# Optimization experiments

Hardware: AMD Instinct MI355X
Metric: run time of the kernel (lower is better)

The kernel has to match this reference:

```python
import jax, jax.numpy as jnp
import numpy as np

N = 100000   # nodes
E = 1600000  # edges
F = 128      # node_feature_dim
H = 128      # hidden_dim
O = 256      # output_dim
G = 256      # number of graphs in the batch


def setup_inputs() -> dict:
    key = jax.random.key(0)
    ks = jax.random.split(key, 12)
    x = jax.random.normal(ks[0], (N, F), dtype=jnp.float32)
    edge_index = jax.random.randint(ks[1], (2, E), 0, N, dtype=jnp.int64)
    batch = jnp.sort(jax.random.randint(ks[2], (N,), 0, G, dtype=jnp.int64))

    def lin(k, fan_in, shape):
        return (jax.random.normal(k, shape, dtype=jnp.float32) / np.float32(np.sqrt(fan_in)))

    W1 = lin(ks[3], F, (F, H)); b1 = jnp.zeros((H,), jnp.float32)
    W2 = lin(ks[4], H, (H, H)); b2 = jnp.zeros((H,), jnp.float32)
    W3 = lin(ks[5], H, (H, H)); b3 = jnp.zeros((H,), jnp.float32)
    Wfc = lin(ks[6], H, (H, O))
    bfc = lin(ks[7], H, (O,))
    return {"x": x, "W1": W1, "b1": b1, "W2": W2, "b2": b2,
            "W3": W3, "b3": b3, "Wfc": Wfc, "bfc": bfc,
            "edge_index": edge_index, "batch": batch}


def _gcn_norm(edge_index, n_nodes):
    # PyG GCNConv default: add self-loops, symmetric normalization.
    loop = jnp.arange(n_nodes, dtype=edge_index.dtype)
    row = jnp.concatenate([edge_index[0], loop])  # source
    col = jnp.concatenate([edge_index[1], loop])  # target
    deg = jax.ops.segment_sum(jnp.ones_like(col, dtype=jnp.float32), col,
                              num_segments=n_nodes)
    dinv = jnp.where(deg > 0, jax.lax.rsqrt(deg), 0.0)
    norm = dinv[row] * dinv[col]  # [E+N]
    return row, col, norm


def _gcn_conv(x, W, b, row, col, norm, n_nodes):
    h = x @ W                                   # transform first (PyG order)
    msg = norm[:, None] * h[row]                # gather + scale
    out = jax.ops.segment_sum(msg, col, num_segments=n_nodes)  # scatter-add
    return out + b


def reference(x, W1, b1, W2, b2, W3, b3, Wfc, bfc, edge_index, batch):
    n_nodes = x.shape[0]
    row, col, norm = _gcn_norm(edge_index, n_nodes)
    h = jax.nn.relu(_gcn_conv(x, W1, b1, row, col, norm, n_nodes))
    h = jax.nn.relu(_gcn_conv(h, W2, b2, row, col, norm, n_nodes))
    h = jax.nn.relu(_gcn_conv(h, W3, b3, row, col, norm, n_nodes))
    # global_mean_pool over graph ids
    sums = jax.ops.segment_sum(h, batch, num_segments=G)
    cnt = jax.ops.segment_sum(jnp.ones((n_nodes,), jnp.float32), batch,
                              num_segments=G)
    pooled = sums / jnp.maximum(cnt, 1.0)[:, None]
    return pooled @ Wfc + bfc
```

## Files before the change

### kernel.cpp

```cpp
#include <hip/hip_runtime.h>

#define NF 128
#define NH 128
#define NO 256
#define NG 256

typedef unsigned int   u32;
typedef unsigned short u16;
typedef __attribute__((ext_vector_type(8))) short short8;
typedef __attribute__((ext_vector_type(4))) float floatx4;

__device__ __forceinline__ float bflo(u32 g) { return __uint_as_float(g << 16); }
__device__ __forceinline__ float bfhi(u32 g) { return __uint_as_float(g & 0xffff0000u); }
__device__ __forceinline__ u16 f2bf(float x) {
    u32 u = __float_as_uint(x);
    u += 0x7fffu + ((u >> 16) & 1u);
    return (u16)(u >> 16);
}
__device__ __forceinline__ u32 packbf2(float x, float y) {
    u32 ux = __float_as_uint(x); ux += 0x7fffu + ((ux >> 16) & 1u);
    u32 uy = __float_as_uint(y); uy += 0x7fffu + ((uy >> 16) & 1u);
    return (ux >> 16) | (uy & 0xffff0000u);
}


__global__ __launch_bounds__(256) void count_coarse(const int* __restrict__ col, int E,
                                                    int* __restrict__ bucketCnt) {
    __shared__ int h[256];
    int t = threadIdx.x;
    h[t] = 0;
    __syncthreads();
    int base = blockIdx.x * 4096;
    #pragma unroll
    for (int i = 0; i < 16; ++i) {
        int e = base + i * 256 + t;
        if (e < E) atomicAdd(&h[col[e] >> 9], 1);
    }
    __syncthreads();
    if (h[t]) atomicAdd(&bucketCnt[t], h[t]);
}

__global__ void scan_buckets(const int* __restrict__ bucketCnt, int* __restrict__ cbase,
                             int* __restrict__ gcur) {
    __shared__ int sh[256];
    int t = threadIdx.x;
    int v = bucketCnt[t];
    sh[t] = v; __syncthreads();
    for (int d = 1; d < 256; d <<= 1) {
        int x = (t >= d) ? sh[t - d] : 0;
        __syncthreads();
        sh[t] += x;
        __syncthreads();
    }
    cbase[t] = sh[t] - v;
    gcur[t]  = sh[t] - v;
}


__global__ __launch_bounds__(256) void bin_coarse(const int* __restrict__ row,
                                                  const int* __restrict__ col,
                                                  int* __restrict__ gcur,
                                                  u32* __restrict__ coarse, int E) {
    __shared__ u32 cnt[256];
    __shared__ u32 lcur[256];
    __shared__ u32 gbase[256];
    __shared__ u32 sc[256];
    __shared__ u32 packed[4096];
    int t = threadIdx.x;
    int base = blockIdx.x * 4096;
    cnt[t] = 0;
    __syncthreads();

    u32 rv[16], cv[16];
    #pragma unroll
    for (int i = 0; i < 16; ++i) {
        int e = base + i * 256 + t;
        if (e < E) {
            rv[i] = (u32)row[e];
            cv[i] = (u32)col[e];
            atomicAdd(&cnt[cv[i] >> 9], 1u);
        }
    }
    __syncthreads();
    u32 own = cnt[t];
    sc[t] = own; __syncthreads();
    for (int d = 1; d < 256; d <<= 1) {
        u32 x = (t >= d) ? sc[t - d] : 0;
        __syncthreads();
        sc[t] += x;
        __syncthreads();
    }
    u32 excl = sc[t] - own;
    u32 total = sc[255];
    if (own > 0) gbase[t] = (u32)atomicAdd(&gcur[t], (int)own);
    cnt[t]  = excl;
    lcur[t] = excl;
    __syncthreads();

    #pragma unroll
    for (int i = 0; i < 16; ++i) {
        int e = base + i * 256 + t;
        if (e < E) {
            u32 p = atomicAdd(&lcur[cv[i] >> 9], 1u);
            packed[p] = rv[i] | ((cv[i] & 511u) << 17);
        }
    }
    __syncthreads();

    for (u32 i = t; i < total; i += 256) {
        u32 lo = 0, hi = 255;
        while (lo < hi) { u32 mid = (lo + hi + 1) >> 1; if (cnt[mid] <= i) lo = mid; else hi = mid - 1; }
        coarse[gbase[lo] + (i - cnt[lo])] = packed[i];
    }
}


__global__ __launch_bounds__(256) void build_csr_bucket(const u32* __restrict__ coarse,
                                                        const int* __restrict__ cbase,
                                                        const int* __restrict__ bucketCnt,
                                                        u32* __restrict__ srcs,
                                                        int* __restrict__ deg,
                                                        float* __restrict__ dinv,
                                                        int* __restrict__ offs, int N) {
    __shared__ u32 buf[10240];
    __shared__ u32 hist[512];
    __shared__ u32 scn[512];
    __shared__ u32 tmp[512];
    __shared__ u32 cur[512];
    int t = threadIdx.x;
    int b = blockIdx.x;
    int lo = b << 9;
    if (lo >= N) return;
    int cnt  = bucketCnt[b];
    int base = cbase[b];

    for (int j = t; j < 512; j += 256) hist[j] = 0;
    __syncthreads();
    for (int i = t; i < cnt; i += 256) {
        u32 pk = coarse[base + i];
        buf[i] = pk;
        atomicAdd(&hist[pk >> 17], 1u);
    }
    __syncthreads();
    for (int j = t; j < 512; j += 256) scn[j] = hist[j];
    __syncthreads();
    for (int d = 1; d < 512; d <<= 1) {
        for (int j = t; j < 512; j += 256) tmp[j] = (j >= d) ? scn[j - d] : 0u;
        __syncthreads();
        for (int j = t; j < 512; j += 256) scn[j] += tmp[j];
        __syncthreads();
    }
    int hi = min(lo + 512, N) - lo;
    for (int j = t; j < 512; j += 256) {
        u32 excl = scn[j] - hist[j];
        cur[j] = excl;
        if (j < hi) {
            deg[lo + j]  = (int)hist[j];
            dinv[lo + j] = rsqrtf((float)hist[j] + 1.0f);
            offs[lo + j] = base + (int)excl;
        }
    }
    __syncthreads();
    for (int i = t; i < cnt; i += 256) {
        u32 pk = buf[i];
        u32 c = pk >> 17;
        u32 p = atomicAdd(&cur[c], 1u);
        srcs[base + p] = pk & 0x1ffffu;
    }
}


__global__ void cast_w_t3(const float* __restrict__ W1, const float* __restrict__ W2,
                          const float* __restrict__ W3, u16* __restrict__ Wt1,
                          u16* __restrict__ Wt2, u16* __restrict__ Wt3) {
    int idx = blockIdx.x * 256 + threadIdx.x;
    int w = idx >> 14;
    int r = idx & 16383;
    const float* W = (w == 0) ? W1 : (w == 1) ? W2 : W3;
    u16* Wt = (w == 0) ? Wt1 : (w == 1) ? Wt2 : Wt3;
    int k = r >> 7, c = r & 127;
    Wt[c * NF + k] = f2bf(W[r]);
}


__device__ __forceinline__ void gemm_body(u16* As, u16* Wt, const u16* Wtg,
                                          const float* dinv, u16* C, int n,
                                          int node0, int t) {
    const uint4* Wg = (const uint4*)Wtg;
    #pragma unroll
    for (int i = 0; i < 8; ++i) {
        int idx = t + 256 * i;
        int cc = idx >> 4, q = idx & 15;
        *(uint4*)&Wt[cc * 136 + q * 8] = Wg[cc * 16 + q];
    }
    __syncthreads();

    int wv = t >> 6;
    int l  = t & 63;
    int lr = l & 15;
    int lq = l >> 4;

    floatx4 acc[8];
    #pragma unroll
    for (int c = 0; c < 8; ++c) acc[c] = (floatx4){0.f, 0.f, 0.f, 0.f};

    #pragma unroll
    for (int kk = 0; kk < 4; ++kk) {
        short8 af = *(const short8*)&As[(wv * 16 + lr) * 136 + kk * 32 + lq * 8];
        #pragma unroll
        for (int c = 0; c < 8; ++c) {
            short8 bf = *(const short8*)&Wt[(c * 16 + lr) * 136 + kk * 32 + lq * 8];
            acc[c] = __builtin_amdgcn_mfma_f32_16x16x32_bf16(af, bf, acc[c], 0, 0, 0);
        }
    }
    __syncthreads();

    float* Cs = (float*)Wt;
    #pragma unroll
    for (int c = 0; c < 8; ++c)
        #pragma unroll
        for (int r = 0; r < 4; ++r)
            Cs[(wv * 16 + lq * 4 + r) * 132 + c * 16 + lr] = acc[c][r];
    __syncthreads();

    int nd = t >> 2, seg = t & 3;
    if (node0 + nd < n) {
        float di = dinv[node0 + nd];
        const float* src = &Cs[nd * 132 + seg * 32];
        u32 o[16];
        #pragma unroll
        for (int i = 0; i < 16; ++i) o[i] = packbf2(di * src[2 * i], di * src[2 * i + 1]);
        uint4* dst = (uint4*)(C + (size_t)(node0 + nd) * NH + seg * 32);
        dst[0] = make_uint4(o[0],  o[1],  o[2],  o[3]);
        dst[1] = make_uint4(o[4],  o[5],  o[6],  o[7]);
        dst[2] = make_uint4(o[8],  o[9],  o[10], o[11]);
        dst[3] = make_uint4(o[12], o[13], o[14], o[15]);
    }
}

__global__ __launch_bounds__(256) void gemm_mfma(const u16* __restrict__ A,
                                                 const u16* __restrict__ Wtg,
                                                 const float* __restrict__ dinv,
                                                 u16* __restrict__ C, int n) {
    __shared__ u16 As[64 * 136];
    __shared__ u16 Wt[128 * 136];
    int t = threadIdx.x;
    int node0 = blockIdx.x * 64;

    const uint4* Ag = (const uint4*)A;
    #pragma unroll
    for (int i = 0; i < 4; ++i) {
        int idx = t + 256 * i;
        int nd = idx >> 4, q = idx & 15;
        uint4 v = make_uint4(0, 0, 0, 0);
        if (node0 + nd < n) v = Ag[(size_t)(node0 + nd) * 16 + q];
        *(uint4*)&As[nd * 136 + q * 8] = v;
    }
    gemm_body(As, Wt, Wtg, dinv, C, n, node0, t);
}

__global__ __launch_bounds__(256) void gemm_mfma_f32(const float* __restrict__ A,
                                                     const u16* __restrict__ Wtg,
                                                     const float* __restrict__ dinv,
                                                     u16* __restrict__ C, int n) {
    __shared__ u16 As[64 * 136];
    __shared__ u16 Wt[128 * 136];
    int t = threadIdx.x;
    int node0 = blockIdx.x * 64;

    const float4* Ag = (const float4*)A;
    #pragma unroll
    for (int i = 0; i < 8; ++i) {
        int idx = t + 256 * i;
        int nd = idx >> 5, q = idx & 31;
        float4 v = make_float4(0.f, 0.f, 0.f, 0.f);
        if (node0 + nd < n) v = Ag[(size_t)(node0 + nd) * 32 + q];
        uint2 p; p.x = packbf2(v.x, v.y); p.y = packbf2(v.z, v.w);
        *(uint2*)&As[nd * 136 + q * 4] = p;
    }
    gemm_body(As, Wt, Wtg, dinv, C, n, node0, t);
}


__global__ __launch_bounds__(256) void gcn_aggregate(const u16* __restrict__ gtab,
                                                     const u32* __restrict__ srcs,
                                                     const int* __restrict__ offs,
                                                     const int* __restrict__ deg,
                                                     const float* __restrict__ dinv,
                                                     const float* __restrict__ bias,
                                                     u16* __restrict__ outb, int n) {
    int wv = threadIdx.x >> 6;
    int l  = threadIdx.x & 63;
    int node = blockIdx.x * 4 + wv;
    if (node >= n) return;
    int start = offs[node];
    int end   = start + deg[node];
    const u32* rows = (const u32*)gtab;

    float a0 = 0.f, a1 = 0.f;
    int k = start;
    for (; k + 16 <= end; k += 16) {
        u32 gv[16];
        #pragma unroll
        for (int i = 0; i < 16; ++i) {
            u32 s = srcs[k + i];
            gv[i] = rows[(size_t)s * 64 + l];
        }
        #pragma unroll
        for (int i = 0; i < 16; ++i) { a0 += bflo(gv[i]); a1 += bfhi(gv[i]); }
    }
    for (; k + 4 <= end; k += 4) {
        u32 s0 = srcs[k], s1 = srcs[k + 1], s2 = srcs[k + 2], s3 = srcs[k + 3];
        u32 g0 = rows[(size_t)s0 * 64 + l];
        u32 g1 = rows[(size_t)s1 * 64 + l];
        u32 g2 = rows[(size_t)s2 * 64 + l];
        u32 g3 = rows[(size_t)s3 * 64 + l];
        a0 += bflo(g0) + bflo(g1) + bflo(g2) + bflo(g3);
        a1 += bfhi(g0) + bfhi(g1) + bfhi(g2) + bfhi(g3);
    }
    for (; k < end; ++k) {
        u32 g = rows[(size_t)srcs[k] * 64 + l];
        a0 += bflo(g); a1 += bfhi(g);
    }
    u32 gs = rows[(size_t)node * 64 + l];
    a0 += bflo(gs); a1 += bfhi(gs);
    float di = dinv[node];
    float2 bb = *(const float2*)&bias[l * 2];
    a0 = fmaxf(di * a0 + bb.x, 0.f);
    a1 = fmaxf(di * a1 + bb.y, 0.f);
    ((u32*)outb)[(size_t)node * 64 + l] = packbf2(a0, a1);
}


__global__ __launch_bounds__(256) void pool_partial(const u16* __restrict__ h,
                                                    const int* __restrict__ batch,
                                                    float* __restrict__ pooled, int n) {
    int t = threadIdx.x;
    int j = t & 127, half = t >> 7;
    int bs = blockIdx.x * 128;
    int be = min(bs + 128, n);
    float acc = 0.f;
    int cur = -1;
    for (int i = bs + half; i < be; i += 2) {
        int g = batch[i];
        if (g != cur) {
            if (cur >= 0) atomicAdd(&pooled[(size_t)cur * NH + j], acc);
            acc = 0.f; cur = g;
        }
        acc += __uint_as_float((u32)h[(size_t)i * NH + j] << 16);
    }
    if (cur >= 0) atomicAdd(&pooled[(size_t)cur * NH + j], acc);
}


__global__ __launch_bounds__(256) void final_fc(const float* __restrict__ pooled,
                                                const int* __restrict__ batch,
                                                const float* __restrict__ Wfc,
                                                const float* __restrict__ bfc,
                                                float* __restrict__ out, int n) {
    int g = blockIdx.x;
    int tid = threadIdx.x;

    int lo = 0, hi = n;
    while (lo < hi) { int m = (lo + hi) >> 1; if (batch[m] < g) lo = m + 1; else hi = m; }
    int start = lo;
    hi = n;
    while (lo < hi) { int m = (lo + hi) >> 1; if (batch[m] < g + 1) lo = m + 1; else hi = m; }
    int end = lo;

    __shared__ float pr[NH];
    float inv = 1.0f / fmaxf((float)(end - start), 1.0f);
    if (tid < NH) pr[tid] = pooled[(size_t)g * NH + tid] * inv;
    __syncthreads();

    float o = bfc[tid];
    #pragma unroll 8
    for (int k = 0; k < NH; ++k) o += pr[k] * Wfc[(size_t)k * NO + tid];
    out[(size_t)g * NO + tid] = o;
}


extern "C" void kernel_launch(void* const* d_in, const int* in_sizes, int n_in,
                              void* d_out, int out_size, void* d_ws, size_t ws_size,
                              hipStream_t stream) {
    const float* x   = (const float*)d_in[0];
    const float* W1  = (const float*)d_in[1];
    const float* b1  = (const float*)d_in[2];
    const float* W2  = (const float*)d_in[3];
    const float* b2  = (const float*)d_in[4];
    const float* W3  = (const float*)d_in[5];
    const float* b3  = (const float*)d_in[6];
    const float* Wfc = (const float*)d_in[7];
    const float* bfc = (const float*)d_in[8];
    const int*   ei  = (const int*)d_in[9];
    const int*   bat = (const int*)d_in[10];
    float* out = (float*)d_out;

    const int N = in_sizes[0] / NF;
    const int E = in_sizes[9] / 2;
    const int* rowp = ei;
    const int* colp = ei + E;

    char* w = (char*)d_ws;
    u32* srcs    = (u32*)w;                      w += (size_t)E * 4;
    u32* coarse  = (u32*)w;                      w += (size_t)E * 4;
    u16* hA   = (u16*)w;                         w += (size_t)N * NH * 2;
    u16* hB   = (u16*)w;                         w += (size_t)N * NH * 2;
    u16* tmpb = (u16*)w;                         w += (size_t)N * NH * 2;
    u16* Wt1  = (u16*)w;                         w += NF * NH * 2;
    u16* Wt2  = (u16*)w;                         w += NF * NH * 2;
    u16* Wt3  = (u16*)w;                         w += NF * NH * 2;
    float* dinv = (float*)w;                     w += (size_t)N * 4;
    int* degc   = (int*)w;                       w += (size_t)N * 4;
    int* offs   = (int*)w;                       w += (size_t)N * 4;
    float* pooled = (float*)w;                   w += (size_t)NG * NH * 4;
    int* bucketCnt = (int*)w;                    w += 256 * 4;
    int* cbase  = (int*)w;                       w += 256 * 4;
    int* gcur   = (int*)w;                       w += 256 * 4;

    const int TB = 256;
    int gGemm = (N + 63) / 64;
    int gAgg  = (N + 3) / 4;
    int gPool = (N + 127) / 128;
    int NB = (N + 511) >> 9;
    int gBin = (E + 4095) / 4096;

    hipMemsetAsync(pooled, 0, (size_t)NG * NH * 4 + 256 * 4, stream);

    count_coarse<<<gBin, TB, 0, stream>>>(colp, E, bucketCnt);
    scan_buckets<<<1, 256, 0, stream>>>(bucketCnt, cbase, gcur);
    bin_coarse<<<gBin, TB, 0, stream>>>(rowp, colp, gcur, coarse, E);
    build_csr_bucket<<<NB, TB, 0, stream>>>(coarse, cbase, bucketCnt, srcs, degc, dinv, offs, N);

    cast_w_t3<<<192, TB, 0, stream>>>(W1, W2, W3, Wt1, Wt2, Wt3);

    gemm_mfma_f32<<<gGemm, TB, 0, stream>>>(x, Wt1, dinv, tmpb, N);
    gcn_aggregate<<<gAgg, TB, 0, stream>>>(tmpb, srcs, offs, degc, dinv, b1, hB, N);

    gemm_mfma<<<gGemm, TB, 0, stream>>>(hB, Wt2, dinv, tmpb, N);
    gcn_aggregate<<<gAgg, TB, 0, stream>>>(tmpb, srcs, offs, degc, dinv, b2, hA, N);

    gemm_mfma<<<gGemm, TB, 0, stream>>>(hA, Wt3, dinv, tmpb, N);
    gcn_aggregate<<<gAgg, TB, 0, stream>>>(tmpb, srcs, offs, degc, dinv, b3, hB, N);

    pool_partial<<<gPool, TB, 0, stream>>>(hB, bat, pooled, N);
    final_fc<<<NG, NO, 0, stream>>>(pooled, bat, Wfc, bfc, out, N);
}
```

Baseline: 462.1 us.

## Use persistent GEMM blocks with resident weights and merge setup kernels

The GEMM kernels become persistent. A capped grid of blocks loads the transposed bf16 weight tile into shared memory once, then loops over node tiles, and the epilogue reuses the A buffer in two halves. The weight cast kernel is folded into the edge-count kernel, and zeroing of the pooled buffer moves into the scan kernel, cutting launches and memsets. This is meant to avoid reloading weights per 64-node tile and to reduce launch overhead. The cost is less parallelism per launch and extra barriers per tile.

```diff
diff --git a/kernel.cpp b/kernel.cpp
--- a/kernel.cpp
+++ b/kernel.cpp
@@ -24,13 +24,29 @@
 }
 
 
-__global__ __launch_bounds__(256) void count_coarse(const int* __restrict__ col, int E,
+__global__ __launch_bounds__(256) void setup_kernel(const float* __restrict__ W1,
+                                                    const float* __restrict__ W2,
+                                                    const float* __restrict__ W3,
+                                                    u16* __restrict__ Wt1, u16* __restrict__ Wt2,
+                                                    u16* __restrict__ Wt3,
+                                                    const int* __restrict__ col, int E,
                                                     int* __restrict__ bucketCnt) {
+    int b = blockIdx.x;
+    int t = threadIdx.x;
+    if (b < 192) {
+        int idx = b * 256 + t;
+        int w = idx >> 14;
+        int r = idx & 16383;
+        const float* W = (w == 0) ? W1 : (w == 1) ? W2 : W3;
+        u16* Wt = (w == 0) ? Wt1 : (w == 1) ? Wt2 : Wt3;
+        int k = r >> 7, c = r & 127;
+        Wt[c * NF + k] = f2bf(W[r]);
+        return;
+    }
     __shared__ int h[256];
-    int t = threadIdx.x;
     h[t] = 0;
     __syncthreads();
-    int base = blockIdx.x * 4096;
+    int base = (b - 192) * 4096;
     #pragma unroll
     for (int i = 0; i < 16; ++i) {
         int e = base + i * 256 + t;
@@ -41,7 +57,7 @@
 }
 
 __global__ void scan_buckets(const int* __restrict__ bucketCnt, int* __restrict__ cbase,
-                             int* __restrict__ gcur) {
+                             int* __restrict__ gcur, float* __restrict__ pooled) {
     __shared__ int sh[256];
     int t = threadIdx.x;
     int v = bucketCnt[t];
@@ -54,6 +70,10 @@
     }
     cbase[t] = sh[t] - v;
     gcur[t]  = sh[t] - v;
+    float4 z = make_float4(0.f, 0.f, 0.f, 0.f);
+    float4* p4 = (float4*)pooled;
+    #pragma unroll
+    for (int i = 0; i < 32; ++i) p4[i * 256 + t] = z;
 }
 
 
@@ -170,31 +190,8 @@
 }
 
 
-__global__ void cast_w_t3(const float* __restrict__ W1, const float* __restrict__ W2,
-                          const float* __restrict__ W3, u16* __restrict__ Wt1,
-                          u16* __restrict__ Wt2, u16* __restrict__ Wt3) {
-    int idx = blockIdx.x * 256 + threadIdx.x;
-    int w = idx >> 14;
-    int r = idx & 16383;
-    const float* W = (w == 0) ? W1 : (w == 1) ? W2 : W3;
-    u16* Wt = (w == 0) ? Wt1 : (w == 1) ? Wt2 : Wt3;
-    int k = r >> 7, c = r & 127;
-    Wt[c * NF + k] = f2bf(W[r]);
-}
-
-
-__device__ __forceinline__ void gemm_body(u16* As, u16* Wt, const u16* Wtg,
-                                          const float* dinv, u16* C, int n,
-                                          int node0, int t) {
-    const uint4* Wg = (const uint4*)Wtg;
-    #pragma unroll
-    for (int i = 0; i < 8; ++i) {
-        int idx = t + 256 * i;
-        int cc = idx >> 4, q = idx & 15;
-        *(uint4*)&Wt[cc * 136 + q * 8] = Wg[cc * 16 + q];
-    }
-    __syncthreads();
-
+__device__ __forceinline__ void gemm_tile(u16* As, const u16* Wt, const float* dinv,
+                                          u16* C, int n, int node0, int t) {
     int wv = t >> 6;
     int l  = t & 63;
     int lr = l & 15;
@@ -213,72 +210,99 @@
             acc[c] = __builtin_amdgcn_mfma_f32_16x16x32_bf16(af, bf, acc[c], 0, 0, 0);
         }
     }
-    __syncthreads();
-
-    float* Cs = (float*)Wt;
-    #pragma unroll
-    for (int c = 0; c < 8; ++c)
-        #pragma unroll
-        for (int r = 0; r < 4; ++r)
-            Cs[(wv * 16 + lq * 4 + r) * 132 + c * 16 + lr] = acc[c][r];
-    __syncthreads();
-
-    int nd = t >> 2, seg = t & 3;
-    if (node0 + nd < n) {
-        float di = dinv[node0 + nd];
-        const float* src = &Cs[nd * 132 + seg * 32];
-        u32 o[16];
-        #pragma unroll
-        for (int i = 0; i < 16; ++i) o[i] = packbf2(di * src[2 * i], di * src[2 * i + 1]);
-        uint4* dst = (uint4*)(C + (size_t)(node0 + nd) * NH + seg * 32);
-        dst[0] = make_uint4(o[0],  o[1],  o[2],  o[3]);
-        dst[1] = make_uint4(o[4],  o[5],  o[6],  o[7]);
-        dst[2] = make_uint4(o[8],  o[9],  o[10], o[11]);
-        dst[3] = make_uint4(o[12], o[13], o[14], o[15]);
-    }
+
+    float* Cs = (float*)As;
+    #pragma unroll
+    for (int h = 0; h < 2; ++h) {
+        __syncthreads();
+        if ((wv >> 1) == h) {
+            int lrow = (wv & 1) * 16 + lq * 4;
+            #pragma unroll
+            for (int c = 0; c < 8; ++c)
+                #pragma unroll
+                for (int r = 0; r < 4; ++r)
+                    Cs[(lrow + r) * 132 + c * 16 + lr] = acc[c][r];
+        }
+        __syncthreads();
+        int nd = t >> 3, seg = t & 7;
+        int node = node0 + h * 32 + nd;
+        if (node < n) {
+            float di = dinv[node];
+            const float* src = &Cs[nd * 132 + seg * 16];
+            u32 o[8];
+            #pragma unroll
+            for (int i = 0; i < 8; ++i) o[i] = packbf2(di * src[2 * i], di * src[2 * i + 1]);
+            uint4* dst = (uint4*)(C + (size_t)node * NH + seg * 16);
+            dst[0] = make_uint4(o[0], o[1], o[2], o[3]);
+            dst[1] = make_uint4(o[4], o[5], o[6], o[7]);
+        }
+    }
+    __syncthreads();
 }
 
 __global__ __launch_bounds__(256) void gemm_mfma(const u16* __restrict__ A,
                                                  const u16* __restrict__ Wtg,
                                                  const float* __restrict__ dinv,
-                                                 u16* __restrict__ C, int n) {
+                                                 u16* __restrict__ C, int n, int ntiles) {
+    __shared__ u16 Wt[128 * 136];
     __shared__ u16 As[64 * 136];
-    __shared__ u16 Wt[128 * 136];
-    int t = threadIdx.x;
-    int node0 = blockIdx.x * 64;
-
-    const uint4* Ag = (const uint4*)A;
-    #pragma unroll
-    for (int i = 0; i < 4; ++i) {
+    int t = threadIdx.x;
+
+    const uint4* Wg = (const uint4*)Wtg;
+    #pragma unroll
+    for (int i = 0; i < 8; ++i) {
         int idx = t + 256 * i;
-        int nd = idx >> 4, q = idx & 15;
-        uint4 v = make_uint4(0, 0, 0, 0);
-        if (node0 + nd < n) v = Ag[(size_t)(node0 + nd) * 16 + q];
-        *(uint4*)&As[nd * 136 + q * 8] = v;
-    }
-    gemm_body(As, Wt, Wtg, dinv, C, n, node0, t);
+        int cc = idx >> 4, q = idx & 15;
+        *(uint4*)&Wt[cc * 136 + q * 8] = Wg[cc * 16 + q];
+    }
+
+    for (int tile = blockIdx.x; tile < ntiles; tile += gridDim.x) {
+        int node0 = tile * 64;
+        const uint4* Ag = (const uint4*)A;
+        #pragma unroll
+        for (int i = 0; i < 4; ++i) {
+            int idx = t + 256 * i;
+            int nd = idx >> 4, q = idx & 15;
+            uint4 v = make_uint4(0, 0, 0, 0);
+            if (node0 + nd < n) v = Ag[(size_t)(node0 + nd) * 16 + q];
+            *(uint4*)&As[nd * 136 + q * 8] = v;
+        }
+        __syncthreads();
+        gemm_tile(As, Wt, dinv, C, n, node0, t);
+    }
 }
 
 __global__ __launch_bounds__(256) void gemm_mfma_f32(const float* __restrict__ A,
                                                      const u16* __restrict__ Wtg,
                                                      const float* __restrict__ dinv,
-                                                     u16* __restrict__ C, int n) {
+                                                     u16* __restrict__ C, int n, int ntiles) {
+    __shared__ u16 Wt[128 * 136];
     __shared__ u16 As[64 * 136];
-    __shared__ u16 Wt[128 * 136];
-    int t = threadIdx.x;
-    int node0 = blockIdx.x * 64;
-
-    const float4* Ag = (const float4*)A;
+    int t = threadIdx.x;
+
+    const uint4* Wg = (const uint4*)Wtg;
     #pragma unroll
     for (int i = 0; i < 8; ++i) {
         int idx = t + 256 * i;
-        int nd = idx >> 5, q = idx & 31;
-        float4 v = make_float4(0.f, 0.f, 0.f, 0.f);
-        if (node0 + nd < n) v = Ag[(size_t)(node0 + nd) * 32 + q];
-        uint2 p; p.x = packbf2(v.x, v.y); p.y = packbf2(v.z, v.w);
-        *(uint2*)&As[nd * 136 + q * 4] = p;
-    }
-    gemm_body(As, Wt, Wtg, dinv, C, n, node0, t);
+        int cc = idx >> 4, q = idx & 15;
+        *(uint4*)&Wt[cc * 136 + q * 8] = Wg[cc * 16 + q];
+    }
+
+    for (int tile = blockIdx.x; tile < ntiles; tile += gridDim.x) {
+        int node0 = tile * 64;
+        const float4* Ag = (const float4*)A;
+        #pragma unroll
+        for (int i = 0; i < 8; ++i) {
+            int idx = t + 256 * i;
+            int nd = idx >> 5, q = idx & 31;
+            float4 v = make_float4(0.f, 0.f, 0.f, 0.f);
+            if (node0 + nd < n) v = Ag[(size_t)(node0 + nd) * 32 + q];
+            uint2 p; p.x = packbf2(v.x, v.y); p.y = packbf2(v.z, v.w);
+            *(uint2*)&As[nd * 136 + q * 4] = p;
+        }
+        __syncthreads();
+        gemm_tile(As, Wt, dinv, C, n, node0, t);
+    }
 }
 
 
@@ -419,28 +443,27 @@
     int* gcur   = (int*)w;                       w += 256 * 4;
 
     const int TB = 256;
-    int gGemm = (N + 63) / 64;
+    int ntiles = (N + 63) / 64;
+    int gGemmP = (ntiles < 768) ? ntiles : 768;
     int gAgg  = (N + 3) / 4;
     int gPool = (N + 127) / 128;
     int NB = (N + 511) >> 9;
     int gBin = (E + 4095) / 4096;
 
-    hipMemsetAsync(pooled, 0, (size_t)NG * NH * 4 + 256 * 4, stream);
-
-    count_coarse<<<gBin, TB, 0, stream>>>(colp, E, bucketCnt);
-    scan_buckets<<<1, 256, 0, stream>>>(bucketCnt, cbase, gcur);
+    hipMemsetAsync(bucketCnt, 0, 256 * 4, stream);
+
+    setup_kernel<<<192 + gBin, TB, 0, stream>>>(W1, W2, W3, Wt1, Wt2, Wt3, colp, E, bucketCnt);
+    scan_buckets<<<1, 256, 0, stream>>>(bucketCnt, cbase, gcur, pooled);
     bin_coarse<<<gBin, TB, 0, stream>>>(rowp, colp, gcur, coarse, E);
     build_csr_bucket<<<NB, TB, 0, stream>>>(coarse, cbase, bucketCnt, srcs, degc, dinv, offs, N);
 
-    cast_w_t3<<<192, TB, 0, stream>>>(W1, W2, W3, Wt1, Wt2, Wt3);
-
-    gemm_mfma_f32<<<gGemm, TB, 0, stream>>>(x, Wt1, dinv, tmpb, N);
+    gemm_mfma_f32<<<gGemmP, TB, 0, stream>>>(x, Wt1, dinv, tmpb, N, ntiles);
     gcn_aggregate<<<gAgg, TB, 0, stream>>>(tmpb, srcs, offs, degc, dinv, b1, hB, N);
 
-    gemm_mfma<<<gGemm, TB, 0, stream>>>(hB, Wt2, dinv, tmpb, N);
+    gemm_mfma<<<gGemmP, TB, 0, stream>>>(hB, Wt2, dinv, tmpb, N, ntiles);
     gcn_aggregate<<<gAgg, TB, 0, stream>>>(tmpb, srcs, offs, degc, dinv, b2, hA, N);
 
-    gemm_mfma<<<gGemm, TB, 0, stream>>>(hA, Wt3, dinv, tmpb, N);
+    gemm_mfma<<<gGemmP, TB, 0, stream>>>(hA, Wt3, dinv, tmpb, N, ntiles);
     gcn_aggregate<<<gAgg, TB, 0, stream>>>(tmpb, srcs, offs, degc, dinv, b3, hB, N);
 
     pool_partial<<<gPool, TB, 0, stream>>>(hB, bat, pooled, N);
```

Measured after the change: 455.1 us. No clear change (-1.5%).
